# Kernel optimization log

Measured on AMD Instinct MI355X. Metric: run time of the kernel, lower is better.

The kernel has to match this reference:

```python
import jax, jax.numpy as jnp
import numpy as np

HID = 1024   # hidden_dim
H = 16       # num_head
D = 64       # head_dim
W = 64       # window_size (one-sided attention radius)


def setup_inputs() -> dict:
    key = jax.random.key(0)
    ks = jax.random.split(key, 10)
    B, S = 2, 4096
    s = 0.02
    X = jax.random.normal(ks[0], (B, S, HID), jnp.float32)
    mask = jnp.ones((B, S), jnp.float32)
    Wq = jax.random.normal(ks[1], (HID, H * D), jnp.float32) * s
    bq = jnp.zeros((H * D,), jnp.float32)
    Wk = jax.random.normal(ks[2], (HID, H * D), jnp.float32) * s
    bk = jnp.zeros((H * D,), jnp.float32)
    Wv = jax.random.normal(ks[3], (HID, H * D), jnp.float32) * s
    bv = jnp.zeros((H * D,), jnp.float32)
    Wo = jax.random.normal(ks[4], (H * D, HID), jnp.float32) * s
    bo = jnp.zeros((HID,), jnp.float32)
    return dict(X=X, mask=mask, Wq=Wq, bq=bq, Wk=Wk, bk=bk, Wv=Wv, bv=bv, Wo=Wo, bo=bo)


def _chunk3(T, nC):
    # T: [B,H,S,D] -> [B,H,nC,3W,D]: for chunk c, keys of chunks c-1, c, c+1 (zero-padded at ends)
    B, Hh, S, Dd = T.shape
    Tp = jnp.pad(T, ((0, 0), (0, 0), (W, W), (0, 0))).reshape(B, Hh, nC + 2, W, Dd)
    return jnp.concatenate([Tp[:, :, :-2], Tp[:, :, 1:-1], Tp[:, :, 2:]], axis=3)


def reference(X, mask, Wq, bq, Wk, bk, Wv, bv, Wo, bo):
    B, S0, _ = X.shape
    pad = W - S0 % W  # matches torch: always >= 1 (full window if divisible)
    Xp = jnp.pad(X, ((0, 0), (0, pad), (0, 0)))
    mp = jnp.pad(mask, ((0, 0), (0, pad)))  # padded keys masked out
    S = S0 + pad
    nC = S // W

    def proj(Wm, b):
        return (Xp @ Wm + b).reshape(B, S, H, D).transpose(0, 2, 1, 3)  # [B,H,S,D]

    Q, K, V = proj(Wq, bq), proj(Wk, bk), proj(Wv, bv)
    Qc = Q.reshape(B, H, nC, W, D)
    K3 = _chunk3(K, nC)
    V3 = _chunk3(V, nC)

    # banded scores: query i attends keys j with |i - j| <= W
    scores = jnp.einsum('bhcqd,bhckd->bhcqk', Qc, K3) / jnp.asarray(np.sqrt(D), jnp.float32)
    qi = jnp.arange(W)[:, None]
    kj = jnp.arange(3 * W)[None, :]
    band = (kj >= qi) & (kj <= qi + 2 * W)  # [W, 3W]
    m3 = jnp.pad(mp, ((0, 0), (W, W))).reshape(B, nC + 2, W)
    m3 = jnp.concatenate([m3[:, :-2], m3[:, 1:-1], m3[:, 2:]], axis=2)  # [B,nC,3W]
    valid = band[None, None, None, :, :] & (m3[:, None, :, None, :] > 0)
    scores = jnp.where(valid, scores, -1e9)
    A = jax.nn.softmax(scores, axis=-1)
    ctx = jnp.einsum('bhcqk,bhckd->bhcqd', A, V3).reshape(B, H, S, D)
    out = ctx.transpose(0, 2, 1, 3).reshape(B, S, H * D) @ Wo + bo
    return out[:, :S0]
```

## Files before the change

kernel.cpp:

```cpp
#include <hip/hip_runtime.h>

typedef unsigned short u16;
typedef unsigned int u32;
typedef __bf16 bf16x8 __attribute__((ext_vector_type(8)));
typedef u16 u16x8 __attribute__((ext_vector_type(8)));
typedef float floatx4 __attribute__((ext_vector_type(4)));

#define MFMA16(a, b, c) __builtin_amdgcn_mfma_f32_16x16x32_bf16((a), (b), (c), 0, 0, 0)

#define B_ 2
#define S0 4096
#define NH 16
#define HD 64
#define HID 1024

__device__ __forceinline__ float bf2f(u16 u) {
  union { u32 i; float f; } x; x.i = ((u32)u) << 16; return x.f;
}
__device__ __forceinline__ u16 f2bf(float f) {
  union { float f; u32 i; } x; x.f = f;
  u32 r = x.i + 0x7FFFu + ((x.i >> 16) & 1u);
  return (u16)(r >> 16);
}

__global__ __launch_bounds__(256) void convert_x(const float* __restrict__ X,
                                                 u16* __restrict__ dst) {
  int i = (blockIdx.x * 256 + threadIdx.x) * 8;
  u16x8 v;
#pragma unroll
  for (int j = 0; j < 8; j++) v[j] = f2bf(X[i + j]);
  *(u16x8*)(dst + i) = v;
}

__global__ __launch_bounds__(256) void convert_small(
    const float* __restrict__ mask, const float* __restrict__ bq,
    const float* __restrict__ bk, const float* __restrict__ bv,
    const float* __restrict__ bo, u16* __restrict__ cmask,
    u16* __restrict__ cb) {
  int tid = blockIdx.x * 256 + threadIdx.x;
  if (tid < B_ * S0) {
    cmask[tid] = f2bf(mask[tid]);
  } else {
    int j = tid - B_ * S0;
    int seg = j >> 10, idx = j & 1023;
    const float* src = (seg == 0) ? bq : (seg == 1) ? bk : (seg == 2) ? bv : bo;
    cb[seg * 1024 + idx] = f2bf(src[idx]);
  }
}

__global__ __launch_bounds__(256) void transpose4(
    const float* __restrict__ Wq, const float* __restrict__ Wk,
    const float* __restrict__ Wv, const float* __restrict__ Wo,
    u16* __restrict__ WqkvT, u16* __restrict__ WoT) {
  __shared__ u16 tile[64][66];
  int mat = blockIdx.z;
  const float* src = (mat == 0) ? Wq : (mat == 1) ? Wk : (mat == 2) ? Wv : Wo;
  u16* dst = (mat < 3) ? (WqkvT + (size_t)mat * HID * HID) : WoT;
  int t0 = blockIdx.x * 64;
  int c0 = blockIdx.y * 64;
  int tx = threadIdx.x & 63, ty = threadIdx.x >> 6;
#pragma unroll
  for (int i = 0; i < 16; i++) {
    int r = i * 4 + ty;
    tile[r][tx] = f2bf(src[(size_t)(t0 + r) * HID + c0 + tx]);
  }
  __syncthreads();
#pragma unroll
  for (int i = 0; i < 16; i++) {
    int r = i * 4 + ty;
    dst[(size_t)(c0 + r) * HID + t0 + tx] = tile[tx][r];
  }
}

__global__ __launch_bounds__(256) void gemm_bf16_tn(
    const u16* __restrict__ A, const u16* __restrict__ Bt,
    const u16* __restrict__ cb, void* __restrict__ outp, int K, int mode) {
  __shared__ alignas(16) u16 sA[128 * 32];
  __shared__ alignas(16) u16 sB[128 * 32];
  int t = threadIdx.x;
  int wave = t >> 6, lane = t & 63;
  int wm = wave >> 1, wn = wave & 1;
  int quad = lane >> 4, l16 = lane & 15;
  int tile_m = blockIdx.x * 128;
  int tile_n = blockIdx.y * 128;

  floatx4 acc[4][4] = {};

  int srow = wave * 16 + (lane >> 2);
  int scol = (lane & 3) * 8;
  const u16* Ag = A + (size_t)(tile_m + srow) * K + scol;
  const u16* Bg = Bt + (size_t)(tile_n + srow) * K + scol;
  u16* sAp = sA + wave * 512 + lane * 8;
  u16* sBp = sB + wave * 512 + lane * 8;
  size_t half = (size_t)64 * K;

  for (int k0 = 0; k0 < K; k0 += 32) {
    u16x8 va0 = *(const u16x8*)(Ag + k0);
    u16x8 va1 = *(const u16x8*)(Ag + half + k0);
    u16x8 vb0 = *(const u16x8*)(Bg + k0);
    u16x8 vb1 = *(const u16x8*)(Bg + half + k0);
    __syncthreads();
    *(u16x8*)(sAp) = va0;
    *(u16x8*)(sAp + 2048) = va1;
    *(u16x8*)(sBp) = vb0;
    *(u16x8*)(sBp + 2048) = vb1;
    __syncthreads();

    bf16x8 af[4], bfr[4];
#pragma unroll
    for (int mt = 0; mt < 4; mt++)
      af[mt] = *(const bf16x8*)(sA + (wm * 64 + mt * 16 + l16) * 32 + quad * 8);
#pragma unroll
    for (int nt = 0; nt < 4; nt++)
      bfr[nt] = *(const bf16x8*)(sB + (wn * 64 + nt * 16 + l16) * 32 + quad * 8);
#pragma unroll
    for (int mt = 0; mt < 4; mt++)
#pragma unroll
      for (int nt = 0; nt < 4; nt++)
        acc[mt][nt] = MFMA16(af[mt], bfr[nt], acc[mt][nt]);
  }

  if (mode == 0) {
    u16* op = (u16*)outp;
#pragma unroll
    for (int mt = 0; mt < 4; mt++) {
      int row0 = tile_m + wm * 64 + mt * 16 + quad * 4;
      int bb = row0 >> 12;
      int sbase = row0 & (S0 - 1);
#pragma unroll
      for (int nt = 0; nt < 4; nt++) {
        int col = tile_n + wn * 64 + nt * 16 + l16;
        int p = col >> 10;
        int rem = col & 1023;
        float bias = bf2f(cb[p * 1024 + rem]);
        int hh = rem >> 6, dd = rem & 63;
        u16* dp = op + ((size_t)(((p * 2 + bb) * NH + hh)) * S0 + sbase) * HD + dd;
#pragma unroll
        for (int r = 0; r < 4; r++)
          dp[(size_t)r * HD] = f2bf(acc[mt][nt][r] + bias);
      }
    }
  } else {
    float* op = (float*)outp;
#pragma unroll
    for (int mt = 0; mt < 4; mt++) {
      int row0 = tile_m + wm * 64 + mt * 16 + quad * 4;
#pragma unroll
      for (int nt = 0; nt < 4; nt++) {
        int col = tile_n + wn * 64 + nt * 16 + l16;
        float bias = bf2f(cb[3 * 1024 + col]);
        float* dp = op + (size_t)row0 * HID + col;
#pragma unroll
        for (int r = 0; r < 4; r++)
          dp[(size_t)r * HID] = acc[mt][nt][r] + bias;
      }
    }
  }
}

__global__ __launch_bounds__(256) void attn_win(
    const u16* __restrict__ Q, const u16* __restrict__ Kp,
    const u16* __restrict__ Vp, const u16* __restrict__ cmask,
    u16* __restrict__ ctx) {
  __shared__ alignas(16) u16 sVt[64 * 200];
  __shared__ alignas(16) u16 sP[4 * 16 * 200];
  __shared__ u16 sMk[192];

  int bid = blockIdx.x;
  int c = bid & 63;
  int h = (bid >> 6) & 15;
  int b = bid >> 10;
  int t = threadIdx.x;
  int wave = t >> 6, lane = t & 63;
  int quad = lane >> 4, l16 = lane & 15;

  const u16* Qb = Q + (size_t)(b * NH + h) * S0 * HD;
  const u16* Kb = Kp + (size_t)(b * NH + h) * S0 * HD;
  const u16* Vb = Vp + (size_t)(b * NH + h) * S0 * HD;
  int kbase = (c - 1) * 64;

#pragma unroll
  for (int i = 0; i < 48; i++) {
    int e = i * 256 + t;
    int slot = e >> 6, d = e & 63;
    int key = kbase + slot;
    int kc = key < 0 ? 0 : (key > S0 - 1 ? S0 - 1 : key);
    sVt[d * 200 + slot] = Vb[(size_t)kc * HD + d];
  }
  if (t < 192) {
    int j = kbase + t;
    sMk[t] = (j >= 0 && j < S0) ? cmask[(size_t)b * S0 + j] : (u16)0;
  }
  __syncthreads();

  floatx4 sc[12] = {};
  int qrow = c * 64 + wave * 16 + l16;
#pragma unroll
  for (int ks = 0; ks < 2; ks++) {
    bf16x8 aq = *(const bf16x8*)(Qb + (size_t)qrow * HD + ks * 32 + quad * 8);
#pragma unroll
    for (int nt = 0; nt < 12; nt++) {
      int key = kbase + nt * 16 + l16;
      int kc = key < 0 ? 0 : (key > S0 - 1 ? S0 - 1 : key);
      bf16x8 bk = *(const bf16x8*)(Kb + (size_t)kc * HD + ks * 32 + quad * 8);
      sc[nt] = MFMA16(aq, bk, sc[nt]);
    }
  }

  int qrel_base = wave * 16 + quad * 4;
  u16* myP = sP + wave * 16 * 200;
  float kmask[12];
#pragma unroll
  for (int nt = 0; nt < 12; nt++) kmask[nt] = bf2f(sMk[nt * 16 + l16]);

#pragma unroll
  for (int reg = 0; reg < 4; reg++) {
    int qrel = qrel_base + reg;
    float v[12];
    float m = -3e38f;
#pragma unroll
    for (int nt = 0; nt < 12; nt++) {
      int jr = nt * 16 + l16 - 64;
      bool ok = (jr >= qrel - 64) && (jr <= qrel + 64) && (kmask[nt] > 0.f);
      float s = ok ? sc[nt][reg] * 0.125f : -1e30f;
      v[nt] = s;
      m = fmaxf(m, s);
    }
#pragma unroll
    for (int off = 1; off <= 8; off <<= 1) m = fmaxf(m, __shfl_xor(m, off));
    float sum = 0.f;
#pragma unroll
    for (int nt = 0; nt < 12; nt++) {
      float p = __expf(v[nt] - m);
      v[nt] = p;
      sum += p;
    }
#pragma unroll
    for (int off = 1; off <= 8; off <<= 1) sum += __shfl_xor(sum, off);
    float inv = 1.0f / sum;
#pragma unroll
    for (int nt = 0; nt < 12; nt++)
      myP[(quad * 4 + reg) * 200 + nt * 16 + l16] = f2bf(v[nt] * inv);
  }
  __syncthreads();

  floatx4 oc[4] = {};
#pragma unroll
  for (int ks = 0; ks < 6; ks++) {
    bf16x8 ap = *(const bf16x8*)(myP + l16 * 200 + ks * 32 + quad * 8);
#pragma unroll
    for (int nt = 0; nt < 4; nt++) {
      bf16x8 bv = *(const bf16x8*)(sVt + (nt * 16 + l16) * 200 + ks * 32 + quad * 8);
      oc[nt] = MFMA16(ap, bv, oc[nt]);
    }
  }

  int srow = c * 64 + wave * 16 + quad * 4;
#pragma unroll
  for (int nt = 0; nt < 4; nt++) {
    u16* dp = ctx + (size_t)(b * S0 + srow) * HID + h * HD + nt * 16 + l16;
#pragma unroll
    for (int reg = 0; reg < 4; reg++)
      dp[(size_t)reg * HID] = f2bf(oc[nt][reg]);
  }
}

extern "C" void kernel_launch(void* const* d_in, const int* in_sizes, int n_in,
                              void* d_out, int out_size, void* d_ws, size_t ws_size,
                              hipStream_t stream) {
  const float* X = (const float*)d_in[0];
  const float* mask = (const float*)d_in[1];
  const float* Wq = (const float*)d_in[2];
  const float* bq = (const float*)d_in[3];
  const float* Wk = (const float*)d_in[4];
  const float* bk = (const float*)d_in[5];
  const float* Wv = (const float*)d_in[6];
  const float* bv = (const float*)d_in[7];
  const float* Wo = (const float*)d_in[8];
  const float* bo = (const float*)d_in[9];
  char* ws = (char*)d_ws;

  const size_t MB = 1048576;
  u16* cmask = (u16*)(ws + 256);
  u16* cb = (u16*)(ws + 256 + 16384);
  u16* cX = (u16*)(ws + 1 * MB);
  u16* WqkvT = (u16*)(ws + 17 * MB);
  u16* WoT = (u16*)(ws + 23 * MB);
  u16* QKV = (u16*)(ws + 25 * MB);
  u16* CTX = cX;

  const size_t per_qkv = (size_t)B_ * NH * S0 * HD;

  convert_x<<<4096, 256, 0, stream>>>(X, cX);
  convert_small<<<48, 256, 0, stream>>>(mask, bq, bk, bv, bo, cmask, cb);
  transpose4<<<dim3(16, 16, 4), 256, 0, stream>>>(Wq, Wk, Wv, Wo, WqkvT, WoT);
  gemm_bf16_tn<<<dim3(64, 24), 256, 0, stream>>>(cX, WqkvT, cb, QKV, HID, 0);
  attn_win<<<dim3(B_ * NH * 64), 256, 0, stream>>>(QKV, QKV + per_qkv,
                                                   QKV + 2 * per_qkv, cmask, CTX);
  gemm_bf16_tn<<<dim3(64, 8), 256, 0, stream>>>(CTX, WoT, cb, d_out, HID, 1);
}
```

Before: 262.7 us.

## Use direct global-to-LDS loads in GEMM and trim attention key band per wave

The GEMM tile loader now uses global_load_lds so data goes from global memory straight into LDS instead of staging through registers. The windowed attention kernel restricts each wave to the 160 keys its 16 queries can reach (offset by wave*16) rather than all 192, cutting QK and PV MFMAs and softmax work by about a sixth. V is loaded with 16-byte vector reads and transposed into a padded LDS buffer instead of scalar per-element loads. The GEMM change drops register prefetch, so it no longer overlaps global loads with the previous iteration's math.

Result: no change. 261.2 us (-0.6%).

```diff
diff --git a/kernel.cpp b/kernel.cpp
--- a/kernel.cpp
+++ b/kernel.cpp
@@ -21,6 +21,12 @@
   union { float f; u32 i; } x; x.f = f;
   u32 r = x.i + 0x7FFFu + ((x.i >> 16) & 1u);
   return (u16)(r >> 16);
+}
+
+__device__ __forceinline__ void glds16(const u16* g, u16* l) {
+  __builtin_amdgcn_global_load_lds(
+      (const __attribute__((address_space(1))) u32*)g,
+      (__attribute__((address_space(3))) u32*)l, 16, 0, 0);
 }
 
 __global__ __launch_bounds__(256) void convert_x(const float* __restrict__ X,
@@ -90,20 +96,18 @@
   int scol = (lane & 3) * 8;
   const u16* Ag = A + (size_t)(tile_m + srow) * K + scol;
   const u16* Bg = Bt + (size_t)(tile_n + srow) * K + scol;
-  u16* sAp = sA + wave * 512 + lane * 8;
-  u16* sBp = sB + wave * 512 + lane * 8;
+  u16* lA0 = sA + wave * 512;
+  u16* lA1 = sA + 2048 + wave * 512;
+  u16* lB0 = sB + wave * 512;
+  u16* lB1 = sB + 2048 + wave * 512;
   size_t half = (size_t)64 * K;
 
   for (int k0 = 0; k0 < K; k0 += 32) {
-    u16x8 va0 = *(const u16x8*)(Ag + k0);
-    u16x8 va1 = *(const u16x8*)(Ag + half + k0);
-    u16x8 vb0 = *(const u16x8*)(Bg + k0);
-    u16x8 vb1 = *(const u16x8*)(Bg + half + k0);
     __syncthreads();
-    *(u16x8*)(sAp) = va0;
-    *(u16x8*)(sAp + 2048) = va1;
-    *(u16x8*)(sBp) = vb0;
-    *(u16x8*)(sBp + 2048) = vb1;
+    glds16(Ag + k0, lA0);
+    glds16(Ag + half + k0, lA1);
+    glds16(Bg + k0, lB0);
+    glds16(Bg + half + k0, lB1);
     __syncthreads();
 
     bf16x8 af[4], bfr[4];
@@ -162,9 +166,9 @@
     const u16* __restrict__ Q, const u16* __restrict__ Kp,
     const u16* __restrict__ Vp, const u16* __restrict__ cmask,
     u16* __restrict__ ctx) {
-  __shared__ alignas(16) u16 sVt[64 * 200];
+  __shared__ alignas(16) u16 sVt[64 * 208];
   __shared__ alignas(16) u16 sP[4 * 16 * 200];
-  __shared__ u16 sMk[192];
+  __shared__ u16 sMk[208];
 
   int bid = blockIdx.x;
   int c = bid & 63;
@@ -173,6 +177,7 @@
   int t = threadIdx.x;
   int wave = t >> 6, lane = t & 63;
   int quad = lane >> 4, l16 = lane & 15;
+  int koff = wave * 16;
 
   const u16* Qb = Q + (size_t)(b * NH + h) * S0 * HD;
   const u16* Kb = Kp + (size_t)(b * NH + h) * S0 * HD;
@@ -180,27 +185,31 @@
   int kbase = (c - 1) * 64;
 
 #pragma unroll
-  for (int i = 0; i < 48; i++) {
+  for (int i = 0; i < 7; i++) {
     int e = i * 256 + t;
-    int slot = e >> 6, d = e & 63;
-    int key = kbase + slot;
-    int kc = key < 0 ? 0 : (key > S0 - 1 ? S0 - 1 : key);
-    sVt[d * 200 + slot] = Vb[(size_t)kc * HD + d];
-  }
-  if (t < 192) {
+    if (e < 1664) {
+      int slot = e >> 3, d0 = (e & 7) * 8;
+      int key = kbase + slot;
+      int kc = key < 0 ? 0 : (key > S0 - 1 ? S0 - 1 : key);
+      u16x8 v = *(const u16x8*)(Vb + (size_t)kc * HD + d0);
+#pragma unroll
+      for (int j = 0; j < 8; j++) sVt[(d0 + j) * 208 + slot] = v[j];
+    }
+  }
+  if (t < 208) {
     int j = kbase + t;
     sMk[t] = (j >= 0 && j < S0) ? cmask[(size_t)b * S0 + j] : (u16)0;
   }
   __syncthreads();
 
-  floatx4 sc[12] = {};
+  floatx4 sc[10] = {};
   int qrow = c * 64 + wave * 16 + l16;
 #pragma unroll
   for (int ks = 0; ks < 2; ks++) {
     bf16x8 aq = *(const bf16x8*)(Qb + (size_t)qrow * HD + ks * 32 + quad * 8);
 #pragma unroll
-    for (int nt = 0; nt < 12; nt++) {
-      int key = kbase + nt * 16 + l16;
+    for (int nt = 0; nt < 10; nt++) {
+      int key = kbase + koff + nt * 16 + l16;
       int kc = key < 0 ? 0 : (key > S0 - 1 ? S0 - 1 : key);
       bf16x8 bk = *(const bf16x8*)(Kb + (size_t)kc * HD + ks * 32 + quad * 8);
       sc[nt] = MFMA16(aq, bk, sc[nt]);
@@ -209,18 +218,18 @@
 
   int qrel_base = wave * 16 + quad * 4;
   u16* myP = sP + wave * 16 * 200;
-  float kmask[12];
-#pragma unroll
-  for (int nt = 0; nt < 12; nt++) kmask[nt] = bf2f(sMk[nt * 16 + l16]);
+  float kmask[10];
+#pragma unroll
+  for (int nt = 0; nt < 10; nt++) kmask[nt] = bf2f(sMk[koff + nt * 16 + l16]);
 
 #pragma unroll
   for (int reg = 0; reg < 4; reg++) {
     int qrel = qrel_base + reg;
-    float v[12];
+    float v[10];
     float m = -3e38f;
 #pragma unroll
-    for (int nt = 0; nt < 12; nt++) {
-      int jr = nt * 16 + l16 - 64;
+    for (int nt = 0; nt < 10; nt++) {
+      int jr = koff + nt * 16 + l16 - 64;
       bool ok = (jr >= qrel - 64) && (jr <= qrel + 64) && (kmask[nt] > 0.f);
       float s = ok ? sc[nt][reg] * 0.125f : -1e30f;
       v[nt] = s;
@@ -230,7 +239,7 @@
     for (int off = 1; off <= 8; off <<= 1) m = fmaxf(m, __shfl_xor(m, off));
     float sum = 0.f;
 #pragma unroll
-    for (int nt = 0; nt < 12; nt++) {
+    for (int nt = 0; nt < 10; nt++) {
       float p = __expf(v[nt] - m);
       v[nt] = p;
       sum += p;
@@ -239,18 +248,19 @@
     for (int off = 1; off <= 8; off <<= 1) sum += __shfl_xor(sum, off);
     float inv = 1.0f / sum;
 #pragma unroll
-    for (int nt = 0; nt < 12; nt++)
+    for (int nt = 0; nt < 10; nt++)
       myP[(quad * 4 + reg) * 200 + nt * 16 + l16] = f2bf(v[nt] * inv);
   }
   __syncthreads();
 
   floatx4 oc[4] = {};
 #pragma unroll
-  for (int ks = 0; ks < 6; ks++) {
+  for (int ks = 0; ks < 5; ks++) {
     bf16x8 ap = *(const bf16x8*)(myP + l16 * 200 + ks * 32 + quad * 8);
 #pragma unroll
     for (int nt = 0; nt < 4; nt++) {
-      bf16x8 bv = *(const bf16x8*)(sVt + (nt * 16 + l16) * 200 + ks * 32 + quad * 8);
+      bf16x8 bv =
+          *(const bf16x8*)(sVt + (nt * 16 + l16) * 208 + koff + ks * 32 + quad * 8);
       oc[nt] = MFMA16(ap, bv, oc[nt]);
     }
   }
```
